# Optimization experiments

Measured on AMD Instinct MI355X. Metric: run time of the kernel, lower is better.

Reference implementation:

```python
import jax, jax.numpy as jnp
import numpy as np

FEAT_DIM = 1280; BD = 256; NH = 4; HD = 64; NQ = 21; NJ = 16
IMG_SIZE = 256.0; GEO_BETA = 1.0; GEO_SIGMA = 0.6; LN_EPS = 1e-5


def _ln(x, g, b):
    m = jnp.mean(x, -1, keepdims=True)
    v = jnp.var(x, -1, keepdims=True)
    return (x - m) * jax.lax.rsqrt(v + LN_EPS) * g + b


def aa_to_rotmat(aa):
    # Rodrigues: aa (..., 3) -> (..., 3, 3)
    ang = jnp.sqrt(jnp.sum(aa * aa, -1, keepdims=True) + 1e-16)
    ax = aa / ang
    x, y, z = ax[..., 0], ax[..., 1], ax[..., 2]
    zero = jnp.zeros_like(x)
    K = jnp.stack([zero, -z, y, z, zero, -x, -y, x, zero], -1).reshape(aa.shape[:-1] + (3, 3))
    s = jnp.sin(ang)[..., None]
    c = jnp.cos(ang)[..., None]
    I = jnp.eye(3, dtype=aa.dtype)
    return I + s * K + (1.0 - c) * jnp.matmul(K, K)


def setup_inputs() -> dict:
    key = jax.random.key(0)
    ks = jax.random.split(key, 20)
    B, H, W = 128, 16, 16
    inp = {}
    inp['img_feat'] = jax.random.normal(ks[0], (B, FEAT_DIM, H, W), jnp.float32)
    inp['joints_3d'] = 0.1 * jax.random.normal(ks[1], (B, NQ, 3), jnp.float32)
    sc = 0.8 + 0.4 * jax.random.uniform(ks[2], (B, 1), jnp.float32)
    txy = 0.05 * jax.random.normal(ks[3], (B, 2), jnp.float32)
    inp['pred_cam'] = jnp.concatenate([sc, txy], -1)
    inp['focal_length'] = 5000.0 * jnp.ones((B, 2), jnp.float32)
    inp['pose_rotmat'] = aa_to_rotmat(0.3 * jax.random.normal(ks[4], (B, NJ, 3), jnp.float32))
    inp['betas'] = 0.1 * jax.random.normal(ks[5], (B, 10), jnp.float32)
    inp['cam'] = jnp.concatenate([sc, txy], -1)

    def lin(k, i, o, std=None):
        s = (1.0 / np.sqrt(i)) if std is None else std
        return (s * jax.random.normal(k, (i, o), jnp.float32)).astype(jnp.float32)

    inp['ln_g'] = jnp.ones((FEAT_DIM,), jnp.float32); inp['ln_b'] = jnp.zeros((FEAT_DIM,), jnp.float32)
    inp['wk'] = lin(ks[6], FEAT_DIM, BD); inp['bk'] = jnp.zeros((BD,), jnp.float32)
    inp['wv'] = lin(ks[7], FEAT_DIM, BD); inp['bv'] = jnp.zeros((BD,), jnp.float32)
    inp['je_w1'] = lin(ks[8], 5, BD); inp['je_b1'] = jnp.zeros((BD,), jnp.float32)
    inp['je_w2'] = lin(ks[9], BD, BD); inp['je_b2'] = jnp.zeros((BD,), jnp.float32)
    inp['joint_id_embed'] = 0.02 * jax.random.normal(ks[10], (1, NQ, BD), jnp.float32)
    inp['wq'] = lin(ks[11], BD, BD); inp['bq'] = jnp.zeros((BD,), jnp.float32)
    inp['wo'] = lin(ks[12], BD, BD); inp['bo'] = jnp.zeros((BD,), jnp.float32)
    inp['norm_g'] = jnp.ones((BD,), jnp.float32); inp['norm_b'] = jnp.zeros((BD,), jnp.float32)
    inp['dec_pose_w'] = lin(ks[13], BD * NQ, 3 * NJ, 1e-4); inp['dec_pose_b'] = jnp.zeros((3 * NJ,), jnp.float32)
    inp['dec_shape_w'] = lin(ks[14], BD, 10, 1e-4); inp['dec_shape_b'] = jnp.zeros((10,), jnp.float32)
    inp['dec_cam_w'] = lin(ks[15], BD, 3, 1e-4); inp['dec_cam_b'] = jnp.zeros((3,), jnp.float32)
    inp['pose_log_scale'] = jnp.float32(-4.0)
    inp['betas_log_scale'] = jnp.float32(-3.0)
    inp['cam_log_scale'] = jnp.float32(-4.0)
    return inp


def reference(img_feat, joints_3d, pred_cam, focal_length, pose_rotmat, betas, cam,
              ln_g, ln_b, wk, bk, wv, bv, je_w1, je_b1, je_w2, je_b2, joint_id_embed,
              wq, bq, wo, bo, norm_g, norm_b, dec_pose_w, dec_pose_b, dec_shape_w,
              dec_shape_b, dec_cam_w, dec_cam_b, pose_log_scale, betas_log_scale, cam_log_scale):
    B, C, H, W = img_feat.shape
    N = H * W
    tokens = img_feat.reshape(B, C, N).transpose(0, 2, 1)        # (B, N, C)
    tokens = _ln(tokens, ln_g, ln_b)
    K = tokens @ wk + bk                                         # (B, N, BD)
    V = tokens @ wv + bv
    patch_h = IMG_SIZE
    patch_w = IMG_SIZE * (float(W) / float(H))
    # weak-perspective projection of 3D joints to 2D
    scale, tx, ty = pred_cam[:, 0], pred_cam[:, 1], pred_cam[:, 2]
    tz = 2.0 * focal_length[:, 0] / (patch_h * scale + 1e-9)
    cam_t = jnp.stack([tx, ty, tz], -1)
    jc = joints_3d + cam_t[:, None, :]
    z = jnp.maximum(jc[..., 2:3], 1e-6)
    xy = jc[..., :2] / z
    center = jnp.array([patch_w * 0.5, patch_h * 0.5], img_feat.dtype)
    j2d = xy * focal_length[:, None, :] + center
    j2dn = jnp.stack([j2d[..., 0] / (patch_w * 0.5) - 1.0,
                      j2d[..., 1] / (patch_h * 0.5) - 1.0], -1)   # (B, Q, 2)
    joint_input = jnp.concatenate([joints_3d, j2dn], -1)         # (B, Q, 5)
    joint_feat = jax.nn.relu(joint_input @ je_w1 + je_b1) @ je_w2 + je_b2 + joint_id_embed
    Qh = (joint_feat @ wq + bq).reshape(B, NQ, NH, HD)
    Kh = K.reshape(B, N, NH, HD)
    Vh = V.reshape(B, N, NH, HD)
    logits = jnp.einsum('bqhd,bnhd->bhqn', Qh, Kh) * (HD ** -0.5)
    # geometric distance bias on token grid in [-1, 1]
    yv = (jnp.arange(H, dtype=img_feat.dtype) + 0.5) / H * 2.0 - 1.0
    xv = (jnp.arange(W, dtype=img_feat.dtype) + 0.5) / W * 2.0 - 1.0
    yy, xx = jnp.meshgrid(yv, xv, indexing='ij')
    token_xy = jnp.stack([xx, yy], -1).reshape(N, 2)
    diff = j2dn[:, :, None, :] - token_xy[None, None]            # (B, Q, N, 2)
    dist2 = jnp.sum(diff * diff, -1)
    geo = -dist2 / (2.0 * GEO_SIGMA ** 2)
    logits = logits + (GEO_BETA * geo)[:, None]
    attn = jax.nn.softmax(logits, -1)
    out = jnp.einsum('bhqn,bnhd->bqhd', attn, Vh).reshape(B, NQ, BD)
    out = _ln(out @ wo + bo + joint_feat, norm_g, norm_b)
    delta_pose = (out.reshape(B, -1) @ dec_pose_w + dec_pose_b) * jnp.exp(pose_log_scale)
    delta_betas = (out.mean(1) @ dec_shape_w + dec_shape_b) * jnp.exp(betas_log_scale)
    delta_cam = (out[:, 0] @ dec_cam_w + dec_cam_b) * jnp.exp(cam_log_scale)
    dR = aa_to_rotmat(delta_pose.reshape(B, NJ, 3))
    pose_new = jnp.matmul(dR, pose_rotmat)                       # (B, 16, 3, 3)
    return pose_new, betas + delta_betas, cam + delta_cam
```

## Files before the change

kernel.cpp:

```cpp
#include <hip/hip_runtime.h>
#include <cstdint>
#include <cstddef>

typedef __attribute__((ext_vector_type(4))) float f32x4;

typedef const __attribute__((address_space(1))) void gv_t;
typedef __attribute__((address_space(3))) void lv_t;
#define GLL16(gsrc, ldst) __builtin_amdgcn_global_load_lds((gv_t*)(gsrc), (lv_t*)(ldst), 16, 0, 0)

template<bool HI>
__device__ __forceinline__ unsigned pk_fp8(float a, float b, unsigned old){
  return (unsigned)__builtin_amdgcn_cvt_pk_fp8_f32(a, b, (int)old, HI);
}
__device__ __forceinline__ uint2 pack8_fp8(const float* v){
  unsigned lo = pk_fp8<false>(v[0], v[1], 0u);
  lo = pk_fp8<true>(v[2], v[3], lo);
  unsigned hi = pk_fp8<false>(v[4], v[5], 0u);
  hi = pk_fp8<true>(v[6], v[7], hi);
  return make_uint2(lo, hi);
}
__device__ __forceinline__ unsigned short f2bf(float f){
  unsigned u = __builtin_bit_cast(unsigned, f);
  u += 0x7fffu + ((u >> 16) & 1u);
  return (unsigned short)(u >> 16);
}
__device__ __forceinline__ float bf2f(unsigned short h){
  unsigned u = ((unsigned)h) << 16;
  return __builtin_bit_cast(float, u);
}


__global__ __launch_bounds__(512) void prep_w(const float* __restrict__ wk, const float* __restrict__ wv,
                                              const float* __restrict__ g, const float* __restrict__ bl,
                                              unsigned char* __restrict__ Wb, float* __restrict__ uvP){
  int dd = threadIdx.x;
  int cs = blockIdx.x;
  const float* w = (dd < 256) ? (wk + dd) : (wv + (dd - 256));
  float uu = 0.f, vv = 0.f;
  for (int cb = 0; cb < 80; cb += 8){
    int c0 = cs * 80 + cb;
    float tmp[8];
    #pragma unroll
    for (int i = 0; i < 8; ++i){
      int c = c0 + i;
      float wc = w[(size_t)c * 256];
      float gw = g[c] * wc;
      uu += gw;
      vv += bl[c] * wc;
      tmp[i] = 16.f * gw;
    }
    uint2 pk = pack8_fp8(tmp);
    *(uint2*)(Wb + ((size_t)(c0 >> 3) * 512 + dd) * 8) = pk;
  }
  uvP[(cs * 2 + 0) * 512 + dd] = uu;
  uvP[(cs * 2 + 1) * 512 + dd] = vv;
}

__global__ __launch_bounds__(512) void reduce_uv(const float* __restrict__ uvP,
                                                 const float* __restrict__ bk, const float* __restrict__ bv,
                                                 float* __restrict__ u, float* __restrict__ v){
  int dd = threadIdx.x;
  float su = 0.f, sv = 0.f;
  #pragma unroll
  for (int cs = 0; cs < 16; ++cs){
    su += uvP[(cs * 2 + 0) * 512 + dd];
    sv += uvP[(cs * 2 + 1) * 512 + dd];
  }
  u[dd] = su;
  v[dd] = sv + ((dd < 256) ? bk[dd] : bv[dd - 256]);
}

__global__ __launch_bounds__(1024) void jointk(const float* __restrict__ joints, const float* __restrict__ pcam,
    const float* __restrict__ focal,
    const float* __restrict__ jw1, const float* __restrict__ jb1,
    const float* __restrict__ jw2, const float* __restrict__ jb2,
    const float* __restrict__ jid, const float* __restrict__ wq, const float* __restrict__ bq,
    float* __restrict__ Jf, float* __restrict__ Qw, float* __restrict__ J2){
  __shared__ float ji[21][5];
  __shared__ float hid[21][256];
  __shared__ float jfs[21][256];
  int b = blockIdx.x, t = threadIdx.x;
  int col = t & 255, grp = t >> 8;
  if (t < 21){
    float sc = pcam[b*3], tx = pcam[b*3+1], ty = pcam[b*3+2];
    float f0 = focal[b*2], f1 = focal[b*2+1];
    float tz = 2.f * f0 / (256.f * sc + 1e-9f);
    const float* jp = joints + (size_t)(b*21 + t) * 3;
    float jx = jp[0], jy = jp[1], jz = jp[2];
    float cx = jx + tx, cy = jy + ty, cz = jz + tz;
    float zz = fmaxf(cz, 1e-6f);
    float nx = (cx / zz) * f0 * (1.f/128.f);
    float ny = (cy / zz) * f1 * (1.f/128.f);
    ji[t][0]=jx; ji[t][1]=jy; ji[t][2]=jz; ji[t][3]=nx; ji[t][4]=ny;
    J2[(b*21 + t)*2 + 0] = nx;
    J2[(b*21 + t)*2 + 1] = ny;
  }
  __syncthreads();
  float w1v[5];
  #pragma unroll
  for (int i = 0; i < 5; ++i) w1v[i] = jw1[i*256 + col];
  float b1v = jb1[col];
  #pragma unroll
  for (int jj = 0; jj < 6; ++jj){
    int q = grp + 4*jj;
    if (q < 21){
      float h = b1v;
      #pragma unroll
      for (int i = 0; i < 5; ++i) h += ji[q][i] * w1v[i];
      hid[q][col] = fmaxf(h, 0.f);
    }
  }
  __syncthreads();
  float accq[6];
  float b2v = jb2[col];
  #pragma unroll
  for (int jj = 0; jj < 6; ++jj){
    int q = grp + 4*jj;
    accq[jj] = (q < 21) ? b2v + jid[q*256 + col] : 0.f;
  }
  for (int k = 0; k < 256; k += 4){
    float w0 = jw2[(k+0)*256 + col], w1 = jw2[(k+1)*256 + col];
    float w2 = jw2[(k+2)*256 + col], w3 = jw2[(k+3)*256 + col];
    #pragma unroll
    for (int jj = 0; jj < 6; ++jj){
      int q = grp + 4*jj;
      if (q < 21){
        f32x4 hv = *(const f32x4*)&hid[q][k];
        accq[jj] += hv.x*w0 + hv.y*w1 + hv.z*w2 + hv.w*w3;
      }
    }
  }
  #pragma unroll
  for (int jj = 0; jj < 6; ++jj){
    int q = grp + 4*jj;
    if (q < 21){ jfs[q][col] = accq[jj]; Jf[(size_t)b*5376 + q*256 + col] = accq[jj]; }
  }
  __syncthreads();
  float bqv = bq[col];
  #pragma unroll
  for (int jj = 0; jj < 6; ++jj) accq[jj] = bqv;
  for (int k = 0; k < 256; k += 4){
    float w0 = wq[(k+0)*256 + col], w1 = wq[(k+1)*256 + col];
    float w2 = wq[(k+2)*256 + col], w3 = wq[(k+3)*256 + col];
    #pragma unroll
    for (int jj = 0; jj < 6; ++jj){
      int q = grp + 4*jj;
      if (q < 21){
        f32x4 hv = *(const f32x4*)&jfs[q][k];
        accq[jj] += hv.x*w0 + hv.y*w1 + hv.z*w2 + hv.w*w3;
      }
    }
  }
  #pragma unroll
  for (int jj = 0; jj < 6; ++jj){
    int q = grp + 4*jj;
    if (q < 21) Qw[(size_t)b*5376 + q*256 + col] = accq[jj];
  }
}

__global__ __launch_bounds__(512) void gemm_kv(const unsigned char* __restrict__ Wb,
    const float* __restrict__ img,
    const float* __restrict__ u, const float* __restrict__ v,
    unsigned short* __restrict__ Kt, unsigned short* __restrict__ Vn, int b0){
  __shared__ long As8[4096];
  __shared__ long Bs8[512];
  __shared__ float sums_lds[64][8][2];
  int blk = blockIdx.x;
  int bl = blk >> 2, nblk = blk & 3;
  int bg = b0 + bl;
  int tid = threadIdx.x, lane = tid & 63, wid = tid >> 6;
  int g = lane >> 4, r = lane & 15;
  int kb_t = wid, n_t = lane;
  const float* xcol = img + (size_t)bg * 1280 * 256 + nblk*64 + n_t;

  f32x4 acc[4][4];
  #pragma unroll
  for (int i = 0; i < 4; ++i)
    #pragma unroll
    for (int j = 0; j < 4; ++j) acc[i][j] = f32x4{0.f,0.f,0.f,0.f};
  float s = 0.f, s2 = 0.f;

  for (int ks = 0; ks < 20; ++ks){
    #pragma unroll
    for (int i = 0; i < 4; ++i){
      int sl = wid*4 + i;
      int kb = sl >> 2, q = sl & 3;
      const unsigned char* srcA = Wb + ((size_t)((ks*8 + kb) * 512 + q*128 + lane*2)) * 8;
      GLL16(srcA, (char*)As8 + ((kb*512 + q*128 + lane*2) * 8));
    }
    {
      float t8[8];
      #pragma unroll
      for (int j = 0; j < 8; ++j){
        float val = xcol[(size_t)(ks*64 + kb_t*8 + j) * 256];
        s += val; s2 += val*val;
        t8[j] = val;
      }
      uint2 pk = pack8_fp8(t8);
      int byte = (kb_t*64 + n_t)*8;
      byte ^= ((n_t & 0x30) << 1) ^ ((kb_t & 3) << 3);
      *(uint2*)((char*)Bs8 + byte) = pk;
    }
    __syncthreads();
    #pragma unroll
    for (int kk = 0; kk < 2; ++kk){
      long av[4], bv4[4];
      #pragma unroll
      for (int m = 0; m < 4; ++m) av[m] = As8[(kk*4 + g)*512 + wid*64 + m*16 + r];
      #pragma unroll
      for (int nn = 0; nn < 4; ++nn){
        int kb = kk*4 + g;
        int n = nn*16 + r;
        int byt = (kb*64 + n)*8;
        byt ^= ((n & 0x30) << 1) ^ ((kb & 3) << 3);
        bv4[nn] = *(const long*)((char*)Bs8 + byt);
      }
      #pragma unroll
      for (int m = 0; m < 4; ++m)
        #pragma unroll
        for (int nn = 0; nn < 4; ++nn)
          acc[m][nn] = __builtin_amdgcn_mfma_f32_16x16x32_fp8_fp8(av[m], bv4[nn], acc[m][nn], 0, 0, 0);
    }
    __syncthreads();
  }

  sums_lds[n_t][kb_t][0] = s;
  sums_lds[n_t][kb_t][1] = s2;
  __syncthreads();

  int b256l = bl * 256;
  float mean[4], rstd[4];
  #pragma unroll
  for (int nn = 0; nn < 4; ++nn){
    int n_row = nn*16 + r;
    float ss = 0.f, ss2 = 0.f;
    #pragma unroll
    for (int kbi = 0; kbi < 8; ++kbi){ ss += sums_lds[n_row][kbi][0]; ss2 += sums_lds[n_row][kbi][1]; }
    float m = ss * (1.f/1280.f);
    float var = ss2 * (1.f/1280.f) - m * m;
    mean[nn] = m;
    rstd[nn] = rsqrtf(var + 1e-5f);
  }
  #pragma unroll
  for (int m = 0; m < 4; ++m){
    #pragma unroll
    for (int reg = 0; reg < 4; ++reg){
      int dd = wid*64 + m*16 + g*4 + reg;
      float uu = u[dd], vv = v[dd];
      #pragma unroll
      for (int nn = 0; nn < 4; ++nn){
        int n = nblk*64 + nn*16 + r;
        float val = rstd[nn] * (acc[m][nn][reg] * 0.0625f - mean[nn] * uu) + vv;
        unsigned short hbf = f2bf(val);
        if (dd < 256) Kt[(size_t)(b256l + dd) * 256 + n] = hbf;
        else          Vn[(size_t)(b256l + n) * 256 + (dd - 256)] = hbf;
      }
    }
  }
}

__global__ __launch_bounds__(256) void attnk(const float* __restrict__ Qw, const unsigned short* __restrict__ Kt,
    const unsigned short* __restrict__ Vn, const float* __restrict__ J2, float* __restrict__ AO, int b0){
  __shared__ float Qs[21][64];
  __shared__ float Ls[21][256];
  __shared__ float j2s[21][2];
  int blk = blockIdx.x;
  int xcd = blk & 7, p = blk >> 3;
  int h = p & 3;
  int bl = (p >> 2) * 8 + xcd;
  int bg = b0 + bl;
  int t = threadIdx.x;
  for (int i = t; i < 21*64; i += 256){
    int q = i >> 6, d = i & 63;
    Qs[q][d] = 0.125f * Qw[(size_t)(bg*21 + q) * 256 + h*64 + d];
  }
  if (t < 42) ((float*)j2s)[t] = J2[bg*42 + t];
  __syncthreads();

  int n = t;
  float xn = (float)(n & 15) * 0.125f - 0.9375f;
  float yn = (float)(n >> 4) * 0.125f - 0.9375f;
  float l[21];
  #pragma unroll
  for (int q = 0; q < 21; ++q){
    float dx = j2s[q][0] - xn, dy = j2s[q][1] - yn;
    l[q] = -(dx*dx + dy*dy) * (1.f/0.72f);
  }
  const unsigned short* Kp = Kt + ((size_t)(bl*256) + h*64) * 256 + n;
  for (int d = 0; d < 64; d += 4){
    float k0 = bf2f(Kp[(size_t)(d+0)*256]);
    float k1 = bf2f(Kp[(size_t)(d+1)*256]);
    float k2 = bf2f(Kp[(size_t)(d+2)*256]);
    float k3 = bf2f(Kp[(size_t)(d+3)*256]);
    #pragma unroll
    for (int q = 0; q < 21; ++q){
      f32x4 qv = *(const f32x4*)&Qs[q][d];
      l[q] += qv.x*k0 + qv.y*k1 + qv.z*k2 + qv.w*k3;
    }
  }
  #pragma unroll
  for (int q = 0; q < 21; ++q) Ls[q][n] = l[q];
  __syncthreads();

  int wv_ = t >> 6, lane = t & 63;
  for (int q = wv_; q < 21; q += 4){
    float v0 = Ls[q][lane], v1 = Ls[q][lane+64], v2 = Ls[q][lane+128], v3 = Ls[q][lane+192];
    float mx = fmaxf(fmaxf(v0, v1), fmaxf(v2, v3));
    #pragma unroll
    for (int off = 32; off >= 1; off >>= 1) mx = fmaxf(mx, __shfl_xor(mx, off));
    float e0 = __expf(v0 - mx), e1 = __expf(v1 - mx), e2 = __expf(v2 - mx), e3 = __expf(v3 - mx);
    float ss = e0 + e1 + e2 + e3;
    #pragma unroll
    for (int off = 32; off >= 1; off >>= 1) ss += __shfl_xor(ss, off);
    float inv = 1.f / ss;
    Ls[q][lane] = e0*inv; Ls[q][lane+64] = e1*inv; Ls[q][lane+128] = e2*inv; Ls[q][lane+192] = e3*inv;
  }
  __syncthreads();

  int d = t & 63, grp = t >> 6;
  const unsigned short* Vp = Vn + (size_t)(bl*256) * 256 + h*64 + d;
  float aq[6] = {0.f,0.f,0.f,0.f,0.f,0.f};
  for (int n2b = 0; n2b < 256; n2b += 32){
    float vdec[32];
    #pragma unroll
    for (int i = 0; i < 32; ++i) vdec[i] = bf2f(Vp[(size_t)(n2b + i) * 256]);
    #pragma unroll
    for (int j = 0; j < 6; ++j){
      int q = grp + 4*j;
      if (q < 21){
        float sacc = 0.f;
        #pragma unroll
        for (int i = 0; i < 32; ++i) sacc += Ls[q][n2b + i] * vdec[i];
        aq[j] += sacc;
      }
    }
  }
  #pragma unroll
  for (int j = 0; j < 6; ++j){
    int q = grp + 4*j;
    if (q < 21) AO[(size_t)(bg*21 + q) * 256 + h*64 + d] = aq[j];
  }
}

__global__ __launch_bounds__(1024) void headk(const float* __restrict__ AO, const float* __restrict__ Jf,
    const float* __restrict__ wo, const float* __restrict__ bo,
    const float* __restrict__ ng, const float* __restrict__ nb_,
    const float* __restrict__ dpw, const float* __restrict__ dpb,
    const float* __restrict__ dsw, const float* __restrict__ dsb,
    const float* __restrict__ dcw, const float* __restrict__ dcb,
    const float* __restrict__ pls, const float* __restrict__ bls, const float* __restrict__ cls,
    const float* __restrict__ prot, const float* __restrict__ betas, const float* __restrict__ cam,
    float* __restrict__ out){
  __shared__ float AOs[21][256];
  __shared__ float Os[21][256];
  __shared__ float mst[21], rst[21];
  __shared__ float pp[21][48];
  __shared__ float dp[48];
  __shared__ float mb[256];
  int b = blockIdx.x, t = threadIdx.x;
  int col = t & 255, grp = t >> 8;
  for (int i = t; i < 5376; i += 1024) ((float*)AOs)[i] = AO[(size_t)b*5376 + i];
  __syncthreads();

  float accq[6];
  float bov = bo[col];
  #pragma unroll
  for (int jj = 0; jj < 6; ++jj){
    int q = grp + 4*jj;
    accq[jj] = (q < 21) ? bov + Jf[(size_t)b*5376 + q*256 + col] : 0.f;
  }
  for (int k = 0; k < 256; k += 4){
    float w0 = wo[(k+0)*256 + col], w1 = wo[(k+1)*256 + col];
    float w2 = wo[(k+2)*256 + col], w3 = wo[(k+3)*256 + col];
    #pragma unroll
    for (int jj = 0; jj < 6; ++jj){
      int q = grp + 4*jj;
      if (q < 21){
        f32x4 av = *(const f32x4*)&AOs[q][k];
        accq[jj] += av.x*w0 + av.y*w1 + av.z*w2 + av.w*w3;
      }
    }
  }
  #pragma unroll
  for (int jj = 0; jj < 6; ++jj){
    int q = grp + 4*jj;
    if (q < 21) Os[q][col] = accq[jj];
  }
  __syncthreads();

  int w = t >> 6, lane = t & 63;
  for (int q = w; q < 21; q += 16){
    float v0 = Os[q][lane], v1 = Os[q][lane+64], v2 = Os[q][lane+128], v3 = Os[q][lane+192];
    float s = v0+v1+v2+v3;
    float s2 = v0*v0+v1*v1+v2*v2+v3*v3;
    #pragma unroll
    for (int off = 32; off >= 1; off >>= 1){ s += __shfl_xor(s, off); s2 += __shfl_xor(s2, off); }
    if (lane == 0){
      float m = s * (1.f/256.f);
      float var = s2 * (1.f/256.f) - m*m;
      mst[q] = m; rst[q] = rsqrtf(var + 1e-5f);
    }
  }
  __syncthreads();

  float gg = ng[col], bb = nb_[col];
  #pragma unroll
  for (int jj = 0; jj < 6; ++jj){
    int q = grp + 4*jj;
    if (q < 21) Os[q][col] = (accq[jj] - mst[q]) * rst[q] * gg + bb;
  }
  __syncthreads();

  if (t < 256){
    float s = 0.f;
    #pragma unroll
    for (int q = 0; q < 21; ++q) s += Os[q][t];
    mb[t] = s * (1.f/21.f);
  }
  if (t < 1008){
    int q = t / 48, j = t % 48;
    float a = 0.f;
    for (int k = 0; k < 256; k += 4){
      f32x4 ov = *(const f32x4*)&Os[q][k];
      const float* wp = dpw + (size_t)(q*256 + k) * 48 + j;
      a += ov.x*wp[0] + ov.y*wp[48] + ov.z*wp[96] + ov.w*wp[144];
    }
    pp[q][j] = a;
  }
  __syncthreads();

  float e_p = __expf(pls[0]), e_b = __expf(bls[0]), e_c = __expf(cls[0]);
  if (t < 48){
    float a = dpb[t];
    #pragma unroll
    for (int q = 0; q < 21; ++q) a += pp[q][t];
    dp[t] = a * e_p;
  }
  __syncthreads();

  if (t < 16){
    int j = t;
    float ax = dp[3*j], ay = dp[3*j+1], az = dp[3*j+2];
    float ang = sqrtf(ax*ax + ay*ay + az*az + 1e-16f);
    float inv = 1.f / ang;
    float x = ax*inv, y = ay*inv, z = az*inv;
    float s_ = sinf(ang), c_ = cosf(ang), mc = 1.f - c_;
    float R00 = 1.f - mc*(y*y + z*z), R01 = -s_*z + mc*x*y,      R02 = s_*y + mc*x*z;
    float R10 = s_*z + mc*x*y,        R11 = 1.f - mc*(x*x + z*z), R12 = -s_*x + mc*y*z;
    float R20 = -s_*y + mc*x*z,       R21 = s_*x + mc*y*z,        R22 = 1.f - mc*(x*x + y*y);
    const float* P = prot + (size_t)(b*16 + j) * 9;
    float p0=P[0],p1=P[1],p2=P[2],p3=P[3],p4=P[4],p5=P[5],p6=P[6],p7=P[7],p8=P[8];
    float* o = out + (size_t)(b*16 + j) * 9;
    o[0]=R00*p0 + R01*p3 + R02*p6; o[1]=R00*p1 + R01*p4 + R02*p7; o[2]=R00*p2 + R01*p5 + R02*p8;
    o[3]=R10*p0 + R11*p3 + R12*p6; o[4]=R10*p1 + R11*p4 + R12*p7; o[5]=R10*p2 + R11*p5 + R12*p8;
    o[6]=R20*p0 + R21*p3 + R22*p6; o[7]=R20*p1 + R21*p4 + R22*p7; o[8]=R20*p2 + R21*p5 + R22*p8;
  }
  if (w >= 4 && w < 14){
    int j = w - 4;
    float a = 0.f;
    #pragma unroll
    for (int i = 0; i < 4; ++i){
      int k = lane + 64*i;
      a += mb[k] * dsw[k*10 + j];
    }
    #pragma unroll
    for (int off = 32; off >= 1; off >>= 1) a += __shfl_xor(a, off);
    if (lane == 0) out[18432 + b*10 + j] = betas[b*10 + j] + (a + dsb[j]) * e_b;
  }
  if (w >= 1 && w < 4){
    int j = w - 1;
    float a = 0.f;
    #pragma unroll
    for (int i = 0; i < 4; ++i){
      int k = lane + 64*i;
      a += Os[0][k] * dcw[k*3 + j];
    }
    #pragma unroll
    for (int off = 32; off >= 1; off >>= 1) a += __shfl_xor(a, off);
    if (lane == 0) out[19712 + b*3 + j] = cam[b*3 + j] + (a + dcb[j]) * e_c;
  }
}

extern "C" void kernel_launch(void* const* d_in, const int* in_sizes, int n_in,
                              void* d_out, int out_size, void* d_ws, size_t ws_size,
                              hipStream_t stream) {
  const float* img    = (const float*)d_in[0];
  const float* joints = (const float*)d_in[1];
  const float* pcam   = (const float*)d_in[2];
  const float* focal  = (const float*)d_in[3];
  const float* prot   = (const float*)d_in[4];
  const float* betas  = (const float*)d_in[5];
  const float* cam    = (const float*)d_in[6];
  const float* ln_g   = (const float*)d_in[7];
  const float* ln_b   = (const float*)d_in[8];
  const float* wk     = (const float*)d_in[9];
  const float* bk     = (const float*)d_in[10];
  const float* wv     = (const float*)d_in[11];
  const float* bv     = (const float*)d_in[12];
  const float* jw1    = (const float*)d_in[13];
  const float* jb1    = (const float*)d_in[14];
  const float* jw2    = (const float*)d_in[15];
  const float* jb2    = (const float*)d_in[16];
  const float* jid    = (const float*)d_in[17];
  const float* wq     = (const float*)d_in[18];
  const float* bq     = (const float*)d_in[19];
  const float* wo     = (const float*)d_in[20];
  const float* bo     = (const float*)d_in[21];
  const float* ng     = (const float*)d_in[22];
  const float* nb     = (const float*)d_in[23];
  const float* dpw    = (const float*)d_in[24];
  const float* dpb    = (const float*)d_in[25];
  const float* dsw    = (const float*)d_in[26];
  const float* dsb    = (const float*)d_in[27];
  const float* dcw    = (const float*)d_in[28];
  const float* dcb    = (const float*)d_in[29];
  const float* pls    = (const float*)d_in[30];
  const float* bls    = (const float*)d_in[31];
  const float* cls    = (const float*)d_in[32];

  char* ws = (char*)d_ws;
  float*         uvP = (float*)(ws + 0);
  float*         u   = (float*)(ws + 65536);
  float*         v   = (float*)(ws + 67584);
  unsigned char* Wb  = (unsigned char*)(ws + 69632);
  float*         Jf  = (float*)(ws + 724992);
  float*         Qw  = (float*)(ws + 3477504);
  float*         J2  = (float*)(ws + 6230016);
  float*         AO  = (float*)(ws + 6251520);
  const size_t FIXED = 9004032;

  int NC = 16;
  for (int c = 1; c <= 16; c <<= 1){
    size_t need = FIXED + (size_t)33554432 / c;
    if (need <= ws_size){ NC = c; break; }
  }
  int Bc = 128 / NC;
  size_t kv_bytes = (size_t)16777216 / NC;
  unsigned short* Kt = (unsigned short*)(ws + FIXED);
  unsigned short* Vn = (unsigned short*)(ws + FIXED + kv_bytes);

  float* out = (float*)d_out;

  prep_w   <<<16,  512, 0, stream>>>(wk, wv, ln_g, ln_b, Wb, uvP);
  reduce_uv<<<1,   512, 0, stream>>>(uvP, bk, bv, u, v);
  jointk   <<<128, 1024, 0, stream>>>(joints, pcam, focal, jw1, jb1, jw2, jb2, jid, wq, bq, Jf, Qw, J2);
  for (int c = 0; c < NC; ++c){
    int b0 = c * Bc;
    gemm_kv <<<Bc*4, 512, 0, stream>>>(Wb, img, u, v, Kt, Vn, b0);
    attnk   <<<Bc*4, 256, 0, stream>>>(Qw, Kt, Vn, J2, AO, b0);
  }
  headk    <<<128, 1024, 0, stream>>>(AO, Jf, wo, bo, ng, nb, dpw, dpb, dsw, dsb, dcw, dcb, pls, bls, cls, prot, betas, cam, out);
}
```

Before: 172.8 us.

## Pre-quantize image features to fp8 in a separate pass before KV GEMM

Adds a pass that reads the fp32 image with vectorized loads, converts it to fp8 in the GEMM's k-block layout and computes per-token LayerNorm partial sums. A small stats kernel then reduces these sums to mean and rstd. gemm_kv now loads pre-quantized B tiles with async global-to-LDS copies and uses a doubled K-step (10 iterations instead of 20). This removes the strided scalar fp32 loads and conversion from the GEMM loop, at the cost of two extra launches per chunk and an extra write and read of the fp8 intermediate plus a larger workspace.

```diff
diff --git a/kernel.cpp b/kernel.cpp
--- a/kernel.cpp
+++ b/kernel.cpp
@@ -68,6 +68,64 @@
   }
   u[dd] = su;
   v[dd] = sv + ((dd < 256) ? bk[dd] : bv[dd - 256]);
+}
+
+__global__ __launch_bounds__(256) void pass1t(const float* __restrict__ img, unsigned char* __restrict__ Xb,
+                                              float* __restrict__ sumsP, int b0){
+  __shared__ float sl[256][4][2];
+  int blk = blockIdx.x;
+  int bl = blk / 20, cs = blk % 20;
+  int bg = b0 + bl;
+  int t = threadIdx.x;
+  int nq = t & 63, rg = t >> 6;
+  const float* src = img + (size_t)bg*1280*256 + (size_t)(cs*64 + rg*16)*256 + nq*4;
+  unsigned q[16];
+  float s[4] = {0.f,0.f,0.f,0.f}, s2[4] = {0.f,0.f,0.f,0.f};
+  #pragma unroll
+  for (int k = 0; k < 16; ++k){
+    f32x4 vv = *(const f32x4*)(src + (size_t)k*256);
+    #pragma unroll
+    for (int i = 0; i < 4; ++i){ s[i] += vv[i]; s2[i] += vv[i]*vv[i]; }
+    unsigned lo = pk_fp8<false>(vv.x, vv.y, 0u);
+    q[k] = pk_fp8<true>(vv.z, vv.w, lo);
+  }
+  #pragma unroll
+  for (int o = 0; o < 2; ++o){
+    size_t kb = (size_t)(bl*160 + cs*8 + rg*2 + o);
+    #pragma unroll
+    for (int i = 0; i < 4; ++i){
+      unsigned lo = 0, hi = 0;
+      #pragma unroll
+      for (int j = 0; j < 4; ++j){
+        lo |= ((q[o*8 + j]     >> (8*i)) & 0xffu) << (8*j);
+        hi |= ((q[o*8 + 4 + j] >> (8*i)) & 0xffu) << (8*j);
+      }
+      *(uint2*)(Xb + (kb*256 + nq*4 + i)*8) = make_uint2(lo, hi);
+    }
+  }
+  #pragma unroll
+  for (int i = 0; i < 4; ++i){ sl[nq*4 + i][rg][0] = s[i]; sl[nq*4 + i][rg][1] = s2[i]; }
+  __syncthreads();
+  {
+    int n = t;
+    float ss  = sl[n][0][0] + sl[n][1][0] + sl[n][2][0] + sl[n][3][0];
+    float ss2 = sl[n][0][1] + sl[n][1][1] + sl[n][2][1] + sl[n][3][1];
+    sumsP[((size_t)(bg*256 + n)*20 + cs)*2 + 0] = ss;
+    sumsP[((size_t)(bg*256 + n)*20 + cs)*2 + 1] = ss2;
+  }
+}
+
+__global__ __launch_bounds__(256) void statsk(const float* __restrict__ sumsP, float* __restrict__ mr, int b0){
+  int bg = b0 + blockIdx.x;
+  int n = threadIdx.x;
+  const float* p = sumsP + (size_t)(bg*256 + n)*40;
+  float s = 0.f, s2 = 0.f;
+  #pragma unroll
+  for (int i = 0; i < 20; ++i){ s += p[2*i]; s2 += p[2*i + 1]; }
+  float m = s * (1.f/1280.f);
+  float var = s2 * (1.f/1280.f) - m*m;
+  mr[((size_t)bg*256 + n)*2 + 0] = m;
+  mr[((size_t)bg*256 + n)*2 + 1] = rsqrtf(var + 1e-5f);
 }
 
 __global__ __launch_bounds__(1024) void jointk(const float* __restrict__ joints, const float* __restrict__ pcam,
@@ -159,62 +217,45 @@
 }
 
 __global__ __launch_bounds__(512) void gemm_kv(const unsigned char* __restrict__ Wb,
-    const float* __restrict__ img,
-    const float* __restrict__ u, const float* __restrict__ v,
+    const unsigned char* __restrict__ Xb,
+    const float* __restrict__ mr, const float* __restrict__ u, const float* __restrict__ v,
     unsigned short* __restrict__ Kt, unsigned short* __restrict__ Vn, int b0){
-  __shared__ long As8[4096];
-  __shared__ long Bs8[512];
-  __shared__ float sums_lds[64][8][2];
+  __shared__ long As8[8192];
+  __shared__ long Bs8[1024];
   int blk = blockIdx.x;
   int bl = blk >> 2, nblk = blk & 3;
   int bg = b0 + bl;
   int tid = threadIdx.x, lane = tid & 63, wid = tid >> 6;
   int g = lane >> 4, r = lane & 15;
-  int kb_t = wid, n_t = lane;
-  const float* xcol = img + (size_t)bg * 1280 * 256 + nblk*64 + n_t;
 
   f32x4 acc[4][4];
   #pragma unroll
   for (int i = 0; i < 4; ++i)
     #pragma unroll
     for (int j = 0; j < 4; ++j) acc[i][j] = f32x4{0.f,0.f,0.f,0.f};
-  float s = 0.f, s2 = 0.f;
-
-  for (int ks = 0; ks < 20; ++ks){
-    #pragma unroll
-    for (int i = 0; i < 4; ++i){
-      int sl = wid*4 + i;
-      int kb = sl >> 2, q = sl & 3;
-      const unsigned char* srcA = Wb + ((size_t)((ks*8 + kb) * 512 + q*128 + lane*2)) * 8;
-      GLL16(srcA, (char*)As8 + ((kb*512 + q*128 + lane*2) * 8));
+
+  for (int ks = 0; ks < 10; ++ks){
+    #pragma unroll
+    for (int i = 0; i < 8; ++i){
+      int sl = wid*8 + i;
+      int kb = sl >> 2, qq = sl & 3;
+      const unsigned char* srcA = Wb + ((size_t)((ks*16 + kb) * 512 + qq*128 + lane*2)) * 8;
+      GLL16(srcA, (char*)As8 + (kb*512 + qq*128 + lane*2) * 8);
     }
     {
-      float t8[8];
+      const unsigned char* srcB = Xb + ((size_t)(bl*160 + ks*16 + wid*2 + (lane>>5)) * 256
+                                        + nblk*64 + (lane&31)*2) * 8;
+      GLL16(srcB, (char*)Bs8 + wid*1024);
+    }
+    __syncthreads();
+    #pragma unroll
+    for (int kk = 0; kk < 4; ++kk){
+      long av[4], bv4[4];
+      int kb = kk*4 + g;
       #pragma unroll
-      for (int j = 0; j < 8; ++j){
-        float val = xcol[(size_t)(ks*64 + kb_t*8 + j) * 256];
-        s += val; s2 += val*val;
-        t8[j] = val;
-      }
-      uint2 pk = pack8_fp8(t8);
-      int byte = (kb_t*64 + n_t)*8;
-      byte ^= ((n_t & 0x30) << 1) ^ ((kb_t & 3) << 3);
-      *(uint2*)((char*)Bs8 + byte) = pk;
-    }
-    __syncthreads();
-    #pragma unroll
-    for (int kk = 0; kk < 2; ++kk){
-      long av[4], bv4[4];
+      for (int m = 0; m < 4; ++m) av[m] = As8[kb*512 + wid*64 + m*16 + r];
       #pragma unroll
-      for (int m = 0; m < 4; ++m) av[m] = As8[(kk*4 + g)*512 + wid*64 + m*16 + r];
-      #pragma unroll
-      for (int nn = 0; nn < 4; ++nn){
-        int kb = kk*4 + g;
-        int n = nn*16 + r;
-        int byt = (kb*64 + n)*8;
-        byt ^= ((n & 0x30) << 1) ^ ((kb & 3) << 3);
-        bv4[nn] = *(const long*)((char*)Bs8 + byt);
-      }
+      for (int nn = 0; nn < 4; ++nn) bv4[nn] = Bs8[kb*64 + nn*16 + r];
       #pragma unroll
       for (int m = 0; m < 4; ++m)
         #pragma unroll
@@ -224,22 +265,13 @@
     __syncthreads();
   }
 
-  sums_lds[n_t][kb_t][0] = s;
-  sums_lds[n_t][kb_t][1] = s2;
-  __syncthreads();
-
   int b256l = bl * 256;
   float mean[4], rstd[4];
   #pragma unroll
   for (int nn = 0; nn < 4; ++nn){
-    int n_row = nn*16 + r;
-    float ss = 0.f, ss2 = 0.f;
-    #pragma unroll
-    for (int kbi = 0; kbi < 8; ++kbi){ ss += sums_lds[n_row][kbi][0]; ss2 += sums_lds[n_row][kbi][1]; }
-    float m = ss * (1.f/1280.f);
-    float var = ss2 * (1.f/1280.f) - m * m;
-    mean[nn] = m;
-    rstd[nn] = rsqrtf(var + 1e-5f);
+    int n = nblk*64 + nn*16 + r;
+    mean[nn] = mr[((size_t)bg*256 + n)*2 + 0];
+    rstd[nn] = mr[((size_t)bg*256 + n)*2 + 1];
   }
   #pragma unroll
   for (int m = 0; m < 4; ++m){
@@ -519,25 +551,29 @@
   const float* cls    = (const float*)d_in[32];
 
   char* ws = (char*)d_ws;
-  float*         uvP = (float*)(ws + 0);
-  float*         u   = (float*)(ws + 65536);
-  float*         v   = (float*)(ws + 67584);
-  unsigned char* Wb  = (unsigned char*)(ws + 69632);
-  float*         Jf  = (float*)(ws + 724992);
-  float*         Qw  = (float*)(ws + 3477504);
-  float*         J2  = (float*)(ws + 6230016);
-  float*         AO  = (float*)(ws + 6251520);
-  const size_t FIXED = 9004032;
+  float*         uvP   = (float*)(ws + 0);
+  float*         u     = (float*)(ws + 65536);
+  float*         v     = (float*)(ws + 67584);
+  unsigned char* Wb    = (unsigned char*)(ws + 69632);
+  float*         Jf    = (float*)(ws + 724992);
+  float*         Qw    = (float*)(ws + 3477504);
+  float*         J2    = (float*)(ws + 6230016);
+  float*         AO    = (float*)(ws + 6251520);
+  float*         sumsP = (float*)(ws + 9004032);
+  float*         mr    = (float*)(ws + 14246912);
+  const size_t FIXED = 14509056;
 
   int NC = 16;
   for (int c = 1; c <= 16; c <<= 1){
-    size_t need = FIXED + (size_t)33554432 / c;
+    size_t need = FIXED + (size_t)75497472 / c;
     if (need <= ws_size){ NC = c; break; }
   }
   int Bc = 128 / NC;
+  size_t xb_bytes = (size_t)41943040 / NC;
   size_t kv_bytes = (size_t)16777216 / NC;
-  unsigned short* Kt = (unsigned short*)(ws + FIXED);
-  unsigned short* Vn = (unsigned short*)(ws + FIXED + kv_bytes);
+  unsigned char*  Xb = (unsigned char*)(ws + FIXED);
+  unsigned short* Kt = (unsigned short*)(ws + FIXED + xb_bytes);
+  unsigned short* Vn = (unsigned short*)(ws + FIXED + xb_bytes + kv_bytes);
 
   float* out = (float*)d_out;
 
@@ -546,8 +582,10 @@
   jointk   <<<128, 1024, 0, stream>>>(joints, pcam, focal, jw1, jb1, jw2, jb2, jid, wq, bq, Jf, Qw, J2);
   for (int c = 0; c < NC; ++c){
     int b0 = c * Bc;
-    gemm_kv <<<Bc*4, 512, 0, stream>>>(Wb, img, u, v, Kt, Vn, b0);
-    attnk   <<<Bc*4, 256, 0, stream>>>(Qw, Kt, Vn, J2, AO, b0);
+    pass1t  <<<Bc*20, 256, 0, stream>>>(img, Xb, sumsP, b0);
+    statsk  <<<Bc,    256, 0, stream>>>(sumsP, mr, b0);
+    gemm_kv <<<Bc*4,  512, 0, stream>>>(Wb, Xb, mr, u, v, Kt, Vn, b0);
+    attnk   <<<Bc*4,  256, 0, stream>>>(Qw, Kt, Vn, J2, AO, b0);
   }
   headk    <<<128, 1024, 0, stream>>>(AO, Jf, wo, bo, ng, nb, dpw, dpb, dsw, dsb, dcw, dcb, pls, bls, cls, prot, betas, cam, out);
 }
```

Measured after the change: 214.2 us. 24.0% more time.

## Halve gemm_kv token tile to 32 columns, doubling grid size

Applied to the files above, without the earlier changes.

Splits each batch's 256-token dimension into 8 blocks of 32 columns instead of 4 blocks of 64, so the K/V projection GEMM launches twice as many workgroups. It reorganizes the fp8 B-tile staging (16 row groups of 4 values per thread, a new XOR swizzle), shrinks the accumulators, and adds a launch-bounds occupancy hint. The aim is more parallelism and latency hiding on the memory-bound image read. The cost is that every block reloads the full fp8 weight tile, which doubles weight traffic, and the LayerNorm statistics now reduce over 16 partial sums.

```diff
diff --git a/kernel.cpp b/kernel.cpp
--- a/kernel.cpp
+++ b/kernel.cpp
@@ -158,84 +158,82 @@
   }
 }
 
-__global__ __launch_bounds__(512) void gemm_kv(const unsigned char* __restrict__ Wb,
+__global__ __launch_bounds__(512, 6) void gemm_kv(const unsigned char* __restrict__ Wb,
     const float* __restrict__ img,
     const float* __restrict__ u, const float* __restrict__ v,
     unsigned short* __restrict__ Kt, unsigned short* __restrict__ Vn, int b0){
   __shared__ long As8[4096];
-  __shared__ long Bs8[512];
-  __shared__ float sums_lds[64][8][2];
+  __shared__ long Bs8[256];
+  __shared__ float sums_lds[32][16][2];
   int blk = blockIdx.x;
-  int bl = blk >> 2, nblk = blk & 3;
+  int bl = blk >> 3, nblk = blk & 7;
   int bg = b0 + bl;
   int tid = threadIdx.x, lane = tid & 63, wid = tid >> 6;
   int g = lane >> 4, r = lane & 15;
-  int kb_t = wid, n_t = lane;
-  const float* xcol = img + (size_t)bg * 1280 * 256 + nblk*64 + n_t;
-
-  f32x4 acc[4][4];
-  #pragma unroll
-  for (int i = 0; i < 4; ++i)
-    #pragma unroll
-    for (int j = 0; j < 4; ++j) acc[i][j] = f32x4{0.f,0.f,0.f,0.f};
+  int n_t = tid & 31, rowg = tid >> 5;
+  const float* xcol = img + (size_t)bg * 1280 * 256 + nblk*32 + n_t;
+
+  f32x4 acc[4][2];
+  #pragma unroll
+  for (int i = 0; i < 4; ++i){ acc[i][0] = f32x4{0.f,0.f,0.f,0.f}; acc[i][1] = f32x4{0.f,0.f,0.f,0.f}; }
   float s = 0.f, s2 = 0.f;
+
+  int kbb = rowg >> 1;
+  int wbyte = ((kbb*32 + n_t)*8 + (rowg&1)*4) ^ ((kbb & 3) << 4);
 
   for (int ks = 0; ks < 20; ++ks){
     #pragma unroll
     for (int i = 0; i < 4; ++i){
       int sl = wid*4 + i;
-      int kb = sl >> 2, q = sl & 3;
-      const unsigned char* srcA = Wb + ((size_t)((ks*8 + kb) * 512 + q*128 + lane*2)) * 8;
-      GLL16(srcA, (char*)As8 + ((kb*512 + q*128 + lane*2) * 8));
+      int kb = sl >> 2, qq = sl & 3;
+      const unsigned char* srcA = Wb + ((size_t)((ks*8 + kb) * 512 + qq*128 + lane*2)) * 8;
+      GLL16(srcA, (char*)As8 + (kb*4096 + qq*1024 + lane*16));
     }
     {
-      float t8[8];
+      float t4[4];
       #pragma unroll
-      for (int j = 0; j < 8; ++j){
-        float val = xcol[(size_t)(ks*64 + kb_t*8 + j) * 256];
+      for (int j = 0; j < 4; ++j){
+        float val = xcol[(size_t)(ks*64 + rowg*4 + j) * 256];
         s += val; s2 += val*val;
-        t8[j] = val;
-      }
-      uint2 pk = pack8_fp8(t8);
-      int byte = (kb_t*64 + n_t)*8;
-      byte ^= ((n_t & 0x30) << 1) ^ ((kb_t & 3) << 3);
-      *(uint2*)((char*)Bs8 + byte) = pk;
+        t4[j] = val;
+      }
+      unsigned pk = pk_fp8<false>(t4[0], t4[1], 0u);
+      pk = pk_fp8<true>(t4[2], t4[3], pk);
+      *(unsigned*)((char*)Bs8 + wbyte) = pk;
     }
     __syncthreads();
     #pragma unroll
     for (int kk = 0; kk < 2; ++kk){
-      long av[4], bv4[4];
+      int kb = kk*4 + g;
+      long av[4], bv2[2];
       #pragma unroll
-      for (int m = 0; m < 4; ++m) av[m] = As8[(kk*4 + g)*512 + wid*64 + m*16 + r];
+      for (int m = 0; m < 4; ++m) av[m] = As8[kb*512 + wid*64 + m*16 + r];
       #pragma unroll
-      for (int nn = 0; nn < 4; ++nn){
-        int kb = kk*4 + g;
-        int n = nn*16 + r;
-        int byt = (kb*64 + n)*8;
-        byt ^= ((n & 0x30) << 1) ^ ((kb & 3) << 3);
-        bv4[nn] = *(const long*)((char*)Bs8 + byt);
+      for (int nn = 0; nn < 2; ++nn){
+        int byt = ((kb*32 + nn*16 + r)*8) ^ ((kb & 3) << 4);
+        bv2[nn] = *(const long*)((char*)Bs8 + byt);
       }
       #pragma unroll
       for (int m = 0; m < 4; ++m)
         #pragma unroll
-        for (int nn = 0; nn < 4; ++nn)
-          acc[m][nn] = __builtin_amdgcn_mfma_f32_16x16x32_fp8_fp8(av[m], bv4[nn], acc[m][nn], 0, 0, 0);
+        for (int nn = 0; nn < 2; ++nn)
+          acc[m][nn] = __builtin_amdgcn_mfma_f32_16x16x32_fp8_fp8(av[m], bv2[nn], acc[m][nn], 0, 0, 0);
     }
     __syncthreads();
   }
 
-  sums_lds[n_t][kb_t][0] = s;
-  sums_lds[n_t][kb_t][1] = s2;
+  sums_lds[n_t][rowg][0] = s;
+  sums_lds[n_t][rowg][1] = s2;
   __syncthreads();
 
   int b256l = bl * 256;
-  float mean[4], rstd[4];
-  #pragma unroll
-  for (int nn = 0; nn < 4; ++nn){
+  float mean[2], rstd[2];
+  #pragma unroll
+  for (int nn = 0; nn < 2; ++nn){
     int n_row = nn*16 + r;
     float ss = 0.f, ss2 = 0.f;
     #pragma unroll
-    for (int kbi = 0; kbi < 8; ++kbi){ ss += sums_lds[n_row][kbi][0]; ss2 += sums_lds[n_row][kbi][1]; }
+    for (int rg = 0; rg < 16; ++rg){ ss += sums_lds[n_row][rg][0]; ss2 += sums_lds[n_row][rg][1]; }
     float m = ss * (1.f/1280.f);
     float var = ss2 * (1.f/1280.f) - m * m;
     mean[nn] = m;
@@ -248,8 +246,8 @@
       int dd = wid*64 + m*16 + g*4 + reg;
       float uu = u[dd], vv = v[dd];
       #pragma unroll
-      for (int nn = 0; nn < 4; ++nn){
-        int n = nblk*64 + nn*16 + r;
+      for (int nn = 0; nn < 2; ++nn){
+        int n = nblk*32 + nn*16 + r;
         float val = rstd[nn] * (acc[m][nn][reg] * 0.0625f - mean[nn] * uu) + vv;
         unsigned short hbf = f2bf(val);
         if (dd < 256) Kt[(size_t)(b256l + dd) * 256 + n] = hbf;
@@ -546,7 +544,7 @@
   jointk   <<<128, 1024, 0, stream>>>(joints, pcam, focal, jw1, jb1, jw2, jb2, jid, wq, bq, Jf, Qw, J2);
   for (int c = 0; c < NC; ++c){
     int b0 = c * Bc;
-    gemm_kv <<<Bc*4, 512, 0, stream>>>(Wb, img, u, v, Kt, Vn, b0);
+    gemm_kv <<<Bc*8, 512, 0, stream>>>(Wb, img, u, v, Kt, Vn, b0);
     attnk   <<<Bc*4, 256, 0, stream>>>(Qw, Kt, Vn, J2, AO, b0);
   }
   headk    <<<128, 1024, 0, stream>>>(AO, Jf, wo, bo, ng, nb, dpw, dpb, dsw, dsb, dcw, dcb, pls, bls, cls, prot, betas, cam, out);
```

Result: slower. 188.6 us (+9.2%).
